# Kernel optimization log

Hardware: AMD Instinct MI355X
Metric: run time of the kernel (lower is better)

## Reference

```python
import jax, jax.numpy as jnp
import numpy as np

N_NODES = 50000
N_EDGES = 800000
C = 128
D_IN = 32
T0, T1 = 25000, 25000
OUT = 16


def setup_inputs() -> dict:
    key = jax.random.key(0)
    ks = jax.random.split(key, 16)
    s_in = 1.0 / np.sqrt(D_IN)
    s_c = 1.0 / np.sqrt(C)
    return {
        "feats0": jax.random.normal(ks[0], (T0, D_IN), jnp.float32),
        "feats1": jax.random.normal(ks[1], (T1, D_IN), jnp.float32),
        "enc_w0": jax.random.normal(ks[2], (D_IN, C), jnp.float32) * s_in,
        "enc_b0": jnp.zeros((C,), jnp.float32),
        "enc_w1": jax.random.normal(ks[3], (D_IN, C), jnp.float32) * s_in,
        "enc_b1": jnp.zeros((C,), jnp.float32),
        "w_self0": jax.random.normal(ks[4], (C, C), jnp.float32) * s_c,
        "w_neigh0": jax.random.normal(ks[5], (C, C), jnp.float32) * s_c,
        "b0": jnp.zeros((C,), jnp.float32),
        "w_self1": jax.random.normal(ks[6], (C, C), jnp.float32) * s_c,
        "w_neigh1": jax.random.normal(ks[7], (C, C), jnp.float32) * s_c,
        "b1": jnp.zeros((C,), jnp.float32),
        "head_w": jax.random.normal(ks[8], (C, OUT), jnp.float32) * s_c,
        "head_b": jnp.zeros((OUT,), jnp.float32),
        "node_row_idx": jax.random.randint(ks[9], (N_NODES,), 0, T0 + T1, jnp.int32),
        "edge_index": jax.random.randint(ks[10], (2, N_EDGES), 0, N_NODES, jnp.int32),
    }


def reference(feats0, feats1, enc_w0, enc_b0, enc_w1, enc_b1,
              w_self0, w_neigh0, b0, w_self1, w_neigh1, b1,
              head_w, head_b, node_row_idx, edge_index):
    # Heterogeneous per-table encoding -> [T0+T1, C]
    x0 = feats0 @ enc_w0 + enc_b0
    x1 = feats1 @ enc_w1 + enc_b1
    x_all = jnp.concatenate([x0, x1], axis=0)
    # Irregular gather: each graph node pulls its table row (vectorized form
    # of the Python loop over index_dict/inverse_index_dict in the original)
    x = x_all[node_row_idx]  # [N, C]

    src, dst = edge_index[0], edge_index[1]
    deg = jnp.maximum(
        jax.ops.segment_sum(jnp.ones((N_EDGES,), x.dtype), dst, num_segments=N_NODES),
        1.0)[:, None]

    # GraphSAGE (mean aggr), 2 layers, ReLU between layers
    for ws, wn, bb, act in ((w_self0, w_neigh0, b0, True),
                            (w_self1, w_neigh1, b1, False)):
        agg = jax.ops.segment_sum(x[src], dst, num_segments=N_NODES) / deg
        x = x @ ws + agg @ wn + bb
        if act:
            x = jax.nn.relu(x)

    return x @ head_w + head_b  # [N, OUT]
```

## Files before the change

kernel.cpp:

```cpp
#include <hip/hip_runtime.h>
#include <hip/hip_bf16.h>

#define N_NODES 50000
#define N_EDGES 800000
#define C 128
#define D_IN 32
#define T0 25000
#define OUT_DIM 16
#define NBUCKETS ((N_NODES + 255) / 256)
#define NB1 512
#define CHUNK1 ((N_EDGES + NB1 - 1) / NB1)
#define ENC_BLOCKS 512
#define HIST_BLOCKS 256
#define PREP_ITEMS (2 * 128 * 256 + 2 * 16 * 128)
#define PREP_BLOCKS ((PREP_ITEMS + 255) / 256)


typedef __attribute__((ext_vector_type(8))) short short8;
typedef __attribute__((ext_vector_type(4))) float f32x4;

__device__ __forceinline__ unsigned short f2bf(float f) {
    union { float f; unsigned int i; } u; u.f = f;
    unsigned int x = u.i;
    unsigned int r = x + 0x7fffu + ((x >> 16) & 1u);
    return (unsigned short)(r >> 16);
}
__device__ __forceinline__ float bf2f(unsigned short h) {
    union { unsigned int i; float f; } u; u.i = ((unsigned int)h) << 16;
    return u.f;
}
__device__ __forceinline__ float lo_f(unsigned int w) {
    union { unsigned int i; float f; } u; u.i = w << 16;
    return u.f;
}
__device__ __forceinline__ float hi_f(unsigned int w) {
    union { unsigned int i; float f; } u; u.i = w & 0xffff0000u;
    return u.f;
}
__device__ __forceinline__ void async16(void* lds, const void* g) {
    __builtin_amdgcn_global_load_lds(
        (const __attribute__((address_space(1))) void*)g,
        (__attribute__((address_space(3))) void*)lds, 16, 0, 0);
}
__device__ __forceinline__ void add8(float* a, uint4 v) {
    a[0] += lo_f(v.x); a[1] += hi_f(v.x);
    a[2] += lo_f(v.y); a[3] += hi_f(v.y);
    a[4] += lo_f(v.z); a[5] += hi_f(v.z);
    a[6] += lo_f(v.w); a[7] += hi_f(v.w);
}

__global__ __launch_bounds__(256) void encode_hist_prep_kernel(
    const float* __restrict__ feats0, const float* __restrict__ feats1,
    const float* __restrict__ w0, const float* __restrict__ b0,
    const float* __restrict__ w1, const float* __restrict__ b1,
    const int* __restrict__ row_idx, unsigned short* __restrict__ xh,
    const int* __restrict__ dst, int* __restrict__ bucket_counts,
    const float* __restrict__ ws0, const float* __restrict__ wn0,
    const float* __restrict__ ws1, const float* __restrict__ wn1,
    const float* __restrict__ hw,
    unsigned short* __restrict__ BT0, unsigned short* __restrict__ BT1,
    unsigned short* __restrict__ hwbh, unsigned short* __restrict__ hwbl)
{
    if (blockIdx.x >= ENC_BLOCKS + HIST_BLOCKS) {
        int idx = (blockIdx.x - ENC_BLOCKS - HIST_BLOCKS) * 256 + threadIdx.x;
        const int per_layer = 128 * 256;
        if (idx < 2 * per_layer) {
            int lyr = idx / per_layer;
            int rem = idx - lyr * per_layer;
            int n = rem >> 8;
            int k = rem & 255;
            int seg = k >> 7;
            int ch = k & 127;
            const float* W = (lyr == 0) ? (seg ? wn0 : ws0)
                                        : (seg ? wn1 : ws1);
            (lyr == 0 ? BT0 : BT1)[(size_t)n * 256 + k] =
                f2bf(W[ch * 128 + n]);
            return;
        }
        int jdx = idx - 2 * per_layer;
        if (jdx >= 2 * 16 * 128) return;
        int plane = jdx >> 11;
        int rem = jdx & 2047;
        int n = rem >> 7;
        int k = rem & 127;
        float v = hw[k * OUT_DIM + n];
        unsigned short hi = f2bf(v);
        (plane ? hwbl : hwbh)[n * 136 + k] = plane ? f2bf(v - bf2f(hi)) : hi;
        return;
    }
    if (blockIdx.x >= ENC_BLOCKS) {
        __shared__ int h[NBUCKETS];
        for (int i = threadIdx.x; i < NBUCKETS; i += 256) h[i] = 0;
        __syncthreads();
        int bid = blockIdx.x - ENC_BLOCKS;
        for (int e = bid * 256 + threadIdx.x; e < N_EDGES;
             e += HIST_BLOCKS * 256)
            atomicAdd(&h[dst[e] >> 8], 1);
        __syncthreads();
        for (int i = threadIdx.x; i < NBUCKETS; i += 256)
            if (h[i]) atomicAdd(&bucket_counts[i], h[i]);
        return;
    }

    __shared__ float sw0[D_IN * C];
    __shared__ float sw1[D_IN * C];
    __shared__ float sb0[C];
    __shared__ float sb1[C];
    for (int i = threadIdx.x; i < D_IN * C; i += blockDim.x) {
        sw0[i] = w0[i];
        sw1[i] = w1[i];
    }
    if (threadIdx.x < C) {
        sb0[threadIdx.x] = b0[threadIdx.x];
        sb1[threadIdx.x] = b1[threadIdx.x];
    }
    __syncthreads();

    const int STEP = ENC_BLOCKS * 16;
    int j = threadIdx.x & 15;
    int ln = threadIdx.x >> 4;
    int n = blockIdx.x * 16 + ln;
    int r = (n < N_NODES) ? row_idx[n] : 0;
    for (; n < N_NODES; n += STEP) {
        int nn = n + STEP;
        int rn = (nn < N_NODES) ? row_idx[nn] : 0;
        const float* f = (r < T0) ? (feats0 + (size_t)r * D_IN)
                                  : (feats1 + (size_t)(r - T0) * D_IN);
        const float* W = (r < T0) ? sw0 : sw1;
        const float* B = (r < T0) ? sb0 : sb1;
        float4 f4[8];
#pragma unroll
        for (int i = 0; i < 8; ++i) f4[i] = ((const float4*)f)[i];
        float acc[8];
#pragma unroll
        for (int cc = 0; cc < 8; ++cc) acc[cc] = B[8 * j + cc];
#pragma unroll
        for (int k = 0; k < D_IN; ++k) {
            float fk = ((const float*)f4)[k];
            float4 wa = *(const float4*)&W[k * C + 8 * j];
            float4 wb = *(const float4*)&W[k * C + 8 * j + 4];
            acc[0] += fk * wa.x; acc[1] += fk * wa.y;
            acc[2] += fk * wa.z; acc[3] += fk * wa.w;
            acc[4] += fk * wb.x; acc[5] += fk * wb.y;
            acc[6] += fk * wb.z; acc[7] += fk * wb.w;
        }
        short8 h8;
#pragma unroll
        for (int cc = 0; cc < 8; ++cc) h8[cc] = (short)f2bf(acc[cc]);
        *(short8*)(xh + (size_t)n * 128 + 8 * j) = h8;
        r = rn;
    }
}

__global__ __launch_bounds__(256) void scanb_kernel(
    const int* __restrict__ bucket_counts, int* __restrict__ bucket_base,
    int* __restrict__ bucket_cursor, int* __restrict__ offsets)
{
    __shared__ int ws[4];
    int t = threadIdx.x;
    int c = (t < NBUCKETS) ? bucket_counts[t] : 0;
    int lane = t & 63, wid = t >> 6;
    int v = c;
#pragma unroll
    for (int off = 1; off < 64; off <<= 1) {
        int s = __shfl_up(v, off, 64);
        if (lane >= off) v += s;
    }
    if (lane == 63) ws[wid] = v;
    __syncthreads();
    if (t == 0) {
        int run = 0;
#pragma unroll
        for (int j = 0; j < 4; ++j) { int s = ws[j]; ws[j] = run; run += s; }
    }
    __syncthreads();
    int excl = ws[wid] + (v - c);
    if (t < NBUCKETS) {
        bucket_base[t] = excl;
        bucket_cursor[t] = excl;
    }
    if (t == 0) {
        bucket_base[NBUCKETS] = N_EDGES;
        offsets[N_NODES] = N_EDGES;
    }
}

__global__ __launch_bounds__(256) void bucket1_kernel(
    const int* __restrict__ src, const int* __restrict__ dst,
    int* __restrict__ bucket_cursor, uint2* __restrict__ pairs)
{
    __shared__ int hist[NBUCKETS];
    __shared__ int base[NBUCKETS];
    __shared__ int cur[NBUCKETS];
    int tid = threadIdx.x;
    for (int i = tid; i < NBUCKETS; i += 256) { hist[i] = 0; cur[i] = 0; }
    __syncthreads();
    int ebeg = blockIdx.x * CHUNK1;
    int eend = ebeg + CHUNK1;
    if (eend > N_EDGES) eend = N_EDGES;
    for (int e = ebeg + tid; e < eend; e += 256)
        atomicAdd(&hist[dst[e] >> 8], 1);
    __syncthreads();
    for (int i = tid; i < NBUCKETS; i += 256)
        if (hist[i] > 0) base[i] = atomicAdd(&bucket_cursor[i], hist[i]);
    __syncthreads();
    for (int e = ebeg + tid; e < eend; e += 256) {
        int d = dst[e];
        int b = d >> 8;
        int pos = base[b] + atomicAdd(&cur[b], 1);
        pairs[pos] = make_uint2((unsigned)src[e], (unsigned)d);
    }
}

__global__ __launch_bounds__(256) void bucket2_kernel(
    const uint2* __restrict__ pairs, const int* __restrict__ bucket_base,
    int* __restrict__ offsets, float* __restrict__ deg,
    int* __restrict__ src_sorted)
{
    __shared__ int cnt[256];
    __shared__ int noff[256];
    __shared__ int cur[256];
    __shared__ int ws[4];
    int b = blockIdx.x;
    int n0 = b << 8;
    int tid = threadIdx.x;
    int bb = bucket_base[b];
    int be = bucket_base[b + 1];
    cnt[tid] = 0;
    cur[tid] = 0;
    __syncthreads();
    for (int e = bb + tid; e < be; e += 256)
        atomicAdd(&cnt[pairs[e].y & 255], 1);
    __syncthreads();
    int c = cnt[tid];
    int lane = tid & 63, wid = tid >> 6;
    int v = c;
#pragma unroll
    for (int off = 1; off < 64; off <<= 1) {
        int s = __shfl_up(v, off, 64);
        if (lane >= off) v += s;
    }
    if (lane == 63) ws[wid] = v;
    __syncthreads();
    if (tid == 0) {
        int run = 0;
#pragma unroll
        for (int j = 0; j < 4; ++j) { int s = ws[j]; ws[j] = run; run += s; }
    }
    __syncthreads();
    int o = bb + ws[wid] + (v - c);
    noff[tid] = o;
    int n = n0 + tid;
    if (n < N_NODES) {
        offsets[n] = o;
        deg[n] = (float)(c > 0 ? c : 1);
    }
    __syncthreads();
    for (int e = bb + tid; e < be; e += 256) {
        uint2 p = pairs[e];
        int local = p.y & 255;
        int pos = noff[local] + atomicAdd(&cur[local], 1);
        src_sorted[pos] = (int)p.x;
    }
}

__global__ __launch_bounds__(256) void aggregate_kernel(
    const unsigned short* __restrict__ xh, const int* __restrict__ offsets,
    const int* __restrict__ src_sorted, const float* __restrict__ deg,
    unsigned short* __restrict__ ah)
{
    int wave = (blockIdx.x * blockDim.x + threadIdx.x) >> 6;
    int lane = threadIdx.x & 63;
    if (wave >= N_NODES) return;
    int h = lane >> 4;
    int u = lane & 15;
    int beg = offsets[wave];
    int end = offsets[wave + 1];
    float acc[8];
#pragma unroll
    for (int j = 0; j < 8; ++j) acc[j] = 0.f;

    for (int e = beg; e < end; e += 32) {
        int idx[8], s[8];
#pragma unroll
        for (int t = 0; t < 8; ++t) {
            idx[t] = e + 4 * t + h;
            int cc = idx[t] < end ? idx[t] : beg;
            s[t] = src_sorted[cc];
        }
        uint4 v[8];
#pragma unroll
        for (int t = 0; t < 8; ++t)
            v[t] = *(const uint4*)(xh + (size_t)s[t] * 128 + u * 8);
#pragma unroll
        for (int t = 0; t < 8; ++t)
            if (idx[t] < end) add8(acc, v[t]);
    }

#pragma unroll
    for (int j = 0; j < 8; ++j) {
        acc[j] += __shfl_xor(acc[j], 16);
        acc[j] += __shfl_xor(acc[j], 32);
    }
    if (lane < 16) {
        float inv = 1.0f / deg[wave];
        short8 hv;
#pragma unroll
        for (int j = 0; j < 8; ++j)
            hv[j] = (short)f2bf(acc[j] * inv);
        *(short8*)(ah + (size_t)wave * 128 + u * 8) = hv;
    }
}

#define BM 128
__global__ __launch_bounds__(512) void gemm_mfma(
    unsigned short* __restrict__ xh, const unsigned short* __restrict__ ah,
    const unsigned short* __restrict__ BT, const float* __restrict__ bias,
    int mode,
    const unsigned short* __restrict__ hwbh,
    const unsigned short* __restrict__ hwbl,
    const float* __restrict__ hb, float* __restrict__ out)
{
    __shared__ uint4 smem4[4096];
    char* As = (char*)smem4;
    char* Bs = (char*)smem4 + 32768;
    __shared__ float bias_s[C];
    __shared__ unsigned short hwh_s[16 * 136];
    __shared__ unsigned short hwl_s[16 * 136];
    __shared__ float hb_s[OUT_DIM];

    int tid = threadIdx.x;
    int w = tid >> 6, l = tid & 63;
    int row0 = blockIdx.x * BM;
    if (tid < C) bias_s[tid] = bias[tid];
    if (mode == 2) {
        for (int i = tid; i < 16 * 136; i += 512) {
            hwh_s[i] = hwbh[i];
            hwl_s[i] = hwbl[i];
        }
        if (tid < OUT_DIM) hb_s[tid] = hb[tid];
    }

    f32x4 acc[2][4];
#pragma unroll
    for (int mt = 0; mt < 2; ++mt)
#pragma unroll
        for (int nt = 0; nt < 4; ++nt)
            acc[mt][nt] = (f32x4)(0.f);

    int wm = w & 3;
    int wn = w >> 2;
    int quad = l >> 4;
    int mrow = l & 15;

    for (int c = 0; c < 2; ++c) {
        const char* abase = (const char*)(c == 0 ? xh : ah);
#pragma unroll
        for (int i = 0; i < 4; ++i) {
            int off = i * 8192 + tid * 16;
            int rl = off >> 8;
            int row = row0 + rl;
            if (row > N_NODES - 1) row = N_NODES - 1;
            int u = ((off >> 4) & 15) ^ (rl & 15);
            async16(As + off, abase + (size_t)row * 256 + u * 16);
        }
#pragma unroll
        for (int i = 0; i < 4; ++i) {
            int off = i * 8192 + tid * 16;
            int n = off >> 8;
            int u = ((off >> 4) & 15) ^ (n & 15);
            async16(Bs + off, (const char*)BT + (size_t)n * 512 + c * 256 + u * 16);
        }
        __syncthreads();
#pragma unroll
        for (int ks = 0; ks < 4; ++ks) {
            int cu = ks * 4 + quad;
            int swz = (cu ^ mrow) * 16;
            short8 a0 = *(const short8*)(As + (wm * 32 + mrow) * 256 + swz);
            short8 a1 = *(const short8*)(As + (wm * 32 + 16 + mrow) * 256 + swz);
            short8 b[4];
#pragma unroll
            for (int nt = 0; nt < 4; ++nt)
                b[nt] = *(const short8*)(Bs + (wn * 64 + nt * 16 + mrow) * 256 + swz);
#pragma unroll
            for (int nt = 0; nt < 4; ++nt) {
                acc[0][nt] = __builtin_amdgcn_mfma_f32_16x16x32_bf16(a0, b[nt], acc[0][nt], 0, 0, 0);
                acc[1][nt] = __builtin_amdgcn_mfma_f32_16x16x32_bf16(a1, b[nt], acc[1][nt], 0, 0, 0);
            }
        }
        __syncthreads();
    }

    char* th = (char*)smem4;
    int relu = (mode == 1);
#pragma unroll
    for (int mt = 0; mt < 2; ++mt)
#pragma unroll
        for (int nt = 0; nt < 4; ++nt) {
            int col = wn * 64 + nt * 16 + mrow;
#pragma unroll
            for (int r = 0; r < 4; ++r) {
                int rl = wm * 32 + mt * 16 + quad * 4 + r;
                float v = acc[mt][nt][r] + bias_s[col];
                if (relu) v = fmaxf(v, 0.f);
                int su = (col >> 3) ^ (rl & 15);
                *(unsigned short*)(th + rl * 256 + su * 16 + (col & 7) * 2) =
                    f2bf(v);
            }
        }
    __syncthreads();

    if (mode == 1) {
#pragma unroll
        for (int i = 0; i < 4; ++i) {
            int off = i * 8192 + tid * 16;
            int rl = off >> 8;
            int su = (((off >> 4) & 15) ^ (rl & 15)) * 16;
            int row = row0 + rl;
            if (row < N_NODES)
                *(uint4*)((char*)xh + (size_t)row * 256 + (off & 255)) =
                    *(const uint4*)(th + rl * 256 + su);
        }
    } else {
        f32x4 hacc = (f32x4)(0.f);
        const unsigned short* Bp[2] = {hwh_s, hwl_s};
#pragma unroll
        for (int ps = 0; ps < 2; ++ps) {
#pragma unroll
            for (int ks = 0; ks < 4; ++ks) {
                int su = ((ks * 4 + quad) ^ mrow) * 16;
                short8 a = *(const short8*)(th + (w * 16 + mrow) * 256 + su);
                short8 b = *(const short8*)((const char*)Bp[ps] +
                                            mrow * 272 + ks * 64 + quad * 16);
                hacc = __builtin_amdgcn_mfma_f32_16x16x32_bf16(a, b, hacc, 0, 0, 0);
            }
        }
        float bb = hb_s[mrow];
#pragma unroll
        for (int r = 0; r < 4; ++r) {
            int grow = row0 + w * 16 + quad * 4 + r;
            if (grow < N_NODES)
                out[(size_t)grow * OUT_DIM + mrow] = hacc[r] + bb;
        }
    }
}

extern "C" void kernel_launch(void* const* d_in, const int* in_sizes, int n_in,
                              void* d_out, int out_size, void* d_ws, size_t ws_size,
                              hipStream_t stream)
{
    const float* feats0 = (const float*)d_in[0];
    const float* feats1 = (const float*)d_in[1];
    const float* enc_w0 = (const float*)d_in[2];
    const float* enc_b0 = (const float*)d_in[3];
    const float* enc_w1 = (const float*)d_in[4];
    const float* enc_b1 = (const float*)d_in[5];
    const float* w_self0 = (const float*)d_in[6];
    const float* w_neigh0 = (const float*)d_in[7];
    const float* b0 = (const float*)d_in[8];
    const float* w_self1 = (const float*)d_in[9];
    const float* w_neigh1 = (const float*)d_in[10];
    const float* b1 = (const float*)d_in[11];
    const float* head_w = (const float*)d_in[12];
    const float* head_b = (const float*)d_in[13];
    const int* node_row_idx = (const int*)d_in[14];
    const int* edge_index = (const int*)d_in[15];
    const int* e_src = edge_index;
    const int* e_dst = edge_index + N_EDGES;

    char* p = (char*)d_ws;
    unsigned short* xh = (unsigned short*)p;  p += (size_t)N_NODES * C * 2;
    unsigned short* ah = (unsigned short*)p;  p += (size_t)N_NODES * C * 2;
    unsigned short* BT0 = (unsigned short*)p; p += (size_t)128 * 256 * 2;
    unsigned short* BT1 = (unsigned short*)p; p += (size_t)128 * 256 * 2;
    unsigned short* hwbh = (unsigned short*)p; p += (size_t)16 * 136 * 2;
    unsigned short* hwbl = (unsigned short*)p; p += (size_t)16 * 136 * 2;
    float* deg = (float*)p;        p += (size_t)N_NODES * 4;
    int* offsets = (int*)p;        p += (size_t)(N_NODES + 8) * 4;
    int* bucket_counts = (int*)p;  p += (size_t)(NBUCKETS + 8) * 4;
    int* bucket_base = (int*)p;    p += (size_t)(NBUCKETS + 8) * 4;
    int* bucket_cursor = (int*)p;  p += (size_t)(NBUCKETS + 8) * 4;
    int* src_sorted = (int*)p;     p += (size_t)N_EDGES * 4;
    uint2* pairs = (uint2*)ah;

    hipMemsetAsync(bucket_counts, 0, (size_t)(NBUCKETS + 8) * 4, stream);

    encode_hist_prep_kernel<<<ENC_BLOCKS + HIST_BLOCKS + PREP_BLOCKS, 256, 0,
                              stream>>>(
        feats0, feats1, enc_w0, enc_b0, enc_w1, enc_b1, node_row_idx, xh,
        e_dst, bucket_counts,
        w_self0, w_neigh0, w_self1, w_neigh1, head_w, BT0, BT1, hwbh, hwbl);

    scanb_kernel<<<1, 256, 0, stream>>>(bucket_counts, bucket_base,
                                        bucket_cursor, offsets);
    bucket1_kernel<<<NB1, 256, 0, stream>>>(e_src, e_dst, bucket_cursor, pairs);
    bucket2_kernel<<<NBUCKETS, 256, 0, stream>>>(pairs, bucket_base, offsets,
                                                 deg, src_sorted);

    aggregate_kernel<<<(N_NODES * 64 + 255) / 256, 256, 0, stream>>>(
        xh, offsets, src_sorted, deg, ah);
    gemm_mfma<<<(N_NODES + BM - 1) / BM, 512, 0, stream>>>(
        xh, ah, BT0, b0, 1, hwbh, hwbl, head_b, (float*)d_out);

    aggregate_kernel<<<(N_NODES * 64 + 255) / 256, 256, 0, stream>>>(
        xh, offsets, src_sorted, deg, ah);
    gemm_mfma<<<(N_NODES + BM - 1) / BM, 512, 0, stream>>>(
        xh, ah, BT1, b1, 2, hwbh, hwbl, head_b, (float*)d_out);
}
```

Measured before the change: 226.0 us.

## Fuse neighbor mean aggregation into the SAGE layer GEMM kernel

The separate aggregate kernel is removed. Each GEMM block now gathers and averages neighbor rows for its 128 nodes directly into shared memory, one wave per 16 nodes, then runs the neighbor-weight MFMA followed by the self-weight MFMA. This drops the write and re-read of the aggregated bf16 buffer and two kernel launches. It also double-buffers x (xh to xnew) so blocks never overwrite rows other blocks are still gathering. The trade-off is a gather phase with only 391 blocks and 16 sequential nodes per wave, which may lower latency hiding compared with the one-wave-per-node kernel, and the pairs buffer now takes extra workspace.

```diff
diff --git a/kernel.cpp b/kernel.cpp
--- a/kernel.cpp
+++ b/kernel.cpp
@@ -264,57 +264,11 @@
     }
 }
 
-__global__ __launch_bounds__(256) void aggregate_kernel(
-    const unsigned short* __restrict__ xh, const int* __restrict__ offsets,
-    const int* __restrict__ src_sorted, const float* __restrict__ deg,
-    unsigned short* __restrict__ ah)
-{
-    int wave = (blockIdx.x * blockDim.x + threadIdx.x) >> 6;
-    int lane = threadIdx.x & 63;
-    if (wave >= N_NODES) return;
-    int h = lane >> 4;
-    int u = lane & 15;
-    int beg = offsets[wave];
-    int end = offsets[wave + 1];
-    float acc[8];
-#pragma unroll
-    for (int j = 0; j < 8; ++j) acc[j] = 0.f;
-
-    for (int e = beg; e < end; e += 32) {
-        int idx[8], s[8];
-#pragma unroll
-        for (int t = 0; t < 8; ++t) {
-            idx[t] = e + 4 * t + h;
-            int cc = idx[t] < end ? idx[t] : beg;
-            s[t] = src_sorted[cc];
-        }
-        uint4 v[8];
-#pragma unroll
-        for (int t = 0; t < 8; ++t)
-            v[t] = *(const uint4*)(xh + (size_t)s[t] * 128 + u * 8);
-#pragma unroll
-        for (int t = 0; t < 8; ++t)
-            if (idx[t] < end) add8(acc, v[t]);
-    }
-
-#pragma unroll
-    for (int j = 0; j < 8; ++j) {
-        acc[j] += __shfl_xor(acc[j], 16);
-        acc[j] += __shfl_xor(acc[j], 32);
-    }
-    if (lane < 16) {
-        float inv = 1.0f / deg[wave];
-        short8 hv;
-#pragma unroll
-        for (int j = 0; j < 8; ++j)
-            hv[j] = (short)f2bf(acc[j] * inv);
-        *(short8*)(ah + (size_t)wave * 128 + u * 8) = hv;
-    }
-}
-
 #define BM 128
-__global__ __launch_bounds__(512) void gemm_mfma(
-    unsigned short* __restrict__ xh, const unsigned short* __restrict__ ah,
+__global__ __launch_bounds__(512, 4) void gemm_fused(
+    const unsigned short* __restrict__ xin, unsigned short* __restrict__ xout,
+    const int* __restrict__ offsets, const int* __restrict__ src_sorted,
+    const float* __restrict__ deg,
     const unsigned short* __restrict__ BT, const float* __restrict__ bias,
     int mode,
     const unsigned short* __restrict__ hwbh,
@@ -341,55 +295,122 @@
         if (tid < OUT_DIM) hb_s[tid] = hb[tid];
     }
 
-    f32x4 acc[2][4];
-#pragma unroll
-    for (int mt = 0; mt < 2; ++mt)
-#pragma unroll
-        for (int nt = 0; nt < 4; ++nt)
-            acc[mt][nt] = (f32x4)(0.f);
-
     int wm = w & 3;
     int wn = w >> 2;
     int quad = l >> 4;
     int mrow = l & 15;
-
-    for (int c = 0; c < 2; ++c) {
-        const char* abase = (const char*)(c == 0 ? xh : ah);
-#pragma unroll
-        for (int i = 0; i < 4; ++i) {
-            int off = i * 8192 + tid * 16;
-            int rl = off >> 8;
-            int row = row0 + rl;
-            if (row > N_NODES - 1) row = N_NODES - 1;
-            int u = ((off >> 4) & 15) ^ (rl & 15);
-            async16(As + off, abase + (size_t)row * 256 + u * 16);
-        }
-#pragma unroll
-        for (int i = 0; i < 4; ++i) {
-            int off = i * 8192 + tid * 16;
-            int n = off >> 8;
-            int u = ((off >> 4) & 15) ^ (n & 15);
-            async16(Bs + off, (const char*)BT + (size_t)n * 512 + c * 256 + u * 16);
-        }
-        __syncthreads();
-#pragma unroll
-        for (int ks = 0; ks < 4; ++ks) {
-            int cu = ks * 4 + quad;
-            int swz = (cu ^ mrow) * 16;
-            short8 a0 = *(const short8*)(As + (wm * 32 + mrow) * 256 + swz);
-            short8 a1 = *(const short8*)(As + (wm * 32 + 16 + mrow) * 256 + swz);
-            short8 b[4];
-#pragma unroll
-            for (int nt = 0; nt < 4; ++nt)
-                b[nt] = *(const short8*)(Bs + (wn * 64 + nt * 16 + mrow) * 256 + swz);
-#pragma unroll
-            for (int nt = 0; nt < 4; ++nt) {
-                acc[0][nt] = __builtin_amdgcn_mfma_f32_16x16x32_bf16(a0, b[nt], acc[0][nt], 0, 0, 0);
-                acc[1][nt] = __builtin_amdgcn_mfma_f32_16x16x32_bf16(a1, b[nt], acc[1][nt], 0, 0, 0);
+    int h = l >> 4;
+    int u = l & 15;
+
+#pragma unroll
+    for (int i = 0; i < 4; ++i) {
+        int off = i * 8192 + tid * 16;
+        int n = off >> 8;
+        int uu = ((off >> 4) & 15) ^ (n & 15);
+        async16(Bs + off, (const char*)BT + (size_t)n * 512 + 256 + uu * 16);
+    }
+
+    for (int i = 0; i < 16; ++i) {
+        int rl = w * 16 + i;
+        int node = row0 + rl;
+        if (node > N_NODES - 1) node = N_NODES - 1;
+        int beg = offsets[node];
+        int end = offsets[node + 1];
+        float acc[8];
+#pragma unroll
+        for (int j = 0; j < 8; ++j) acc[j] = 0.f;
+        for (int e = beg; e < end; e += 32) {
+            int idx[8], s[8];
+#pragma unroll
+            for (int t = 0; t < 8; ++t) {
+                idx[t] = e + 4 * t + h;
+                int cc = idx[t] < end ? idx[t] : beg;
+                s[t] = src_sorted[cc];
             }
-        }
-        __syncthreads();
-    }
+            uint4 v[8];
+#pragma unroll
+            for (int t = 0; t < 8; ++t)
+                v[t] = *(const uint4*)(xin + (size_t)s[t] * 128 + u * 8);
+#pragma unroll
+            for (int t = 0; t < 8; ++t)
+                if (idx[t] < end) add8(acc, v[t]);
+        }
+#pragma unroll
+        for (int j = 0; j < 8; ++j) {
+            acc[j] += __shfl_xor(acc[j], 16);
+            acc[j] += __shfl_xor(acc[j], 32);
+        }
+        if (l < 16) {
+            float inv = 1.0f / deg[node];
+            short8 hv;
+#pragma unroll
+            for (int j = 0; j < 8; ++j)
+                hv[j] = (short)f2bf(acc[j] * inv);
+            int su = u ^ (rl & 15);
+            *(short8*)(As + rl * 256 + su * 16) = hv;
+        }
+    }
+    __syncthreads();
+
+    f32x4 acc[2][4];
+#pragma unroll
+    for (int mt = 0; mt < 2; ++mt)
+#pragma unroll
+        for (int nt = 0; nt < 4; ++nt)
+            acc[mt][nt] = (f32x4)(0.f);
+
+#pragma unroll
+    for (int ks = 0; ks < 4; ++ks) {
+        int cu = ks * 4 + quad;
+        int swz = (cu ^ mrow) * 16;
+        short8 a0 = *(const short8*)(As + (wm * 32 + mrow) * 256 + swz);
+        short8 a1 = *(const short8*)(As + (wm * 32 + 16 + mrow) * 256 + swz);
+        short8 b[4];
+#pragma unroll
+        for (int nt = 0; nt < 4; ++nt)
+            b[nt] = *(const short8*)(Bs + (wn * 64 + nt * 16 + mrow) * 256 + swz);
+#pragma unroll
+        for (int nt = 0; nt < 4; ++nt) {
+            acc[0][nt] = __builtin_amdgcn_mfma_f32_16x16x32_bf16(a0, b[nt], acc[0][nt], 0, 0, 0);
+            acc[1][nt] = __builtin_amdgcn_mfma_f32_16x16x32_bf16(a1, b[nt], acc[1][nt], 0, 0, 0);
+        }
+    }
+    __syncthreads();
+
+#pragma unroll
+    for (int i = 0; i < 4; ++i) {
+        int off = i * 8192 + tid * 16;
+        int rl = off >> 8;
+        int row = row0 + rl;
+        if (row > N_NODES - 1) row = N_NODES - 1;
+        int uu = ((off >> 4) & 15) ^ (rl & 15);
+        async16(As + off, (const char*)xin + (size_t)row * 256 + uu * 16);
+    }
+#pragma unroll
+    for (int i = 0; i < 4; ++i) {
+        int off = i * 8192 + tid * 16;
+        int n = off >> 8;
+        int uu = ((off >> 4) & 15) ^ (n & 15);
+        async16(Bs + off, (const char*)BT + (size_t)n * 512 + uu * 16);
+    }
+    __syncthreads();
+#pragma unroll
+    for (int ks = 0; ks < 4; ++ks) {
+        int cu = ks * 4 + quad;
+        int swz = (cu ^ mrow) * 16;
+        short8 a0 = *(const short8*)(As + (wm * 32 + mrow) * 256 + swz);
+        short8 a1 = *(const short8*)(As + (wm * 32 + 16 + mrow) * 256 + swz);
+        short8 b[4];
+#pragma unroll
+        for (int nt = 0; nt < 4; ++nt)
+            b[nt] = *(const short8*)(Bs + (wn * 64 + nt * 16 + mrow) * 256 + swz);
+#pragma unroll
+        for (int nt = 0; nt < 4; ++nt) {
+            acc[0][nt] = __builtin_amdgcn_mfma_f32_16x16x32_bf16(a0, b[nt], acc[0][nt], 0, 0, 0);
+            acc[1][nt] = __builtin_amdgcn_mfma_f32_16x16x32_bf16(a1, b[nt], acc[1][nt], 0, 0, 0);
+        }
+    }
+    __syncthreads();
 
     char* th = (char*)smem4;
     int relu = (mode == 1);
@@ -418,7 +439,7 @@
             int su = (((off >> 4) & 15) ^ (rl & 15)) * 16;
             int row = row0 + rl;
             if (row < N_NODES)
-                *(uint4*)((char*)xh + (size_t)row * 256 + (off & 255)) =
+                *(uint4*)((char*)xout + (size_t)row * 256 + (off & 255)) =
                     *(const uint4*)(th + rl * 256 + su);
         }
     } else {
@@ -469,10 +490,10 @@
     const int* e_dst = edge_index + N_EDGES;
 
     char* p = (char*)d_ws;
-    unsigned short* xh = (unsigned short*)p;  p += (size_t)N_NODES * C * 2;
-    unsigned short* ah = (unsigned short*)p;  p += (size_t)N_NODES * C * 2;
-    unsigned short* BT0 = (unsigned short*)p; p += (size_t)128 * 256 * 2;
-    unsigned short* BT1 = (unsigned short*)p; p += (size_t)128 * 256 * 2;
+    unsigned short* xh = (unsigned short*)p;   p += (size_t)N_NODES * C * 2;
+    unsigned short* xnew = (unsigned short*)p; p += (size_t)N_NODES * C * 2;
+    unsigned short* BT0 = (unsigned short*)p;  p += (size_t)128 * 256 * 2;
+    unsigned short* BT1 = (unsigned short*)p;  p += (size_t)128 * 256 * 2;
     unsigned short* hwbh = (unsigned short*)p; p += (size_t)16 * 136 * 2;
     unsigned short* hwbl = (unsigned short*)p; p += (size_t)16 * 136 * 2;
     float* deg = (float*)p;        p += (size_t)N_NODES * 4;
@@ -481,7 +502,7 @@
     int* bucket_base = (int*)p;    p += (size_t)(NBUCKETS + 8) * 4;
     int* bucket_cursor = (int*)p;  p += (size_t)(NBUCKETS + 8) * 4;
     int* src_sorted = (int*)p;     p += (size_t)N_EDGES * 4;
-    uint2* pairs = (uint2*)ah;
+    uint2* pairs = (uint2*)p;      p += (size_t)N_EDGES * 8;
 
     hipMemsetAsync(bucket_counts, 0, (size_t)(NBUCKETS + 8) * 4, stream);
 
@@ -497,13 +518,11 @@
     bucket2_kernel<<<NBUCKETS, 256, 0, stream>>>(pairs, bucket_base, offsets,
                                                  deg, src_sorted);
 
-    aggregate_kernel<<<(N_NODES * 64 + 255) / 256, 256, 0, stream>>>(
-        xh, offsets, src_sorted, deg, ah);
-    gemm_mfma<<<(N_NODES + BM - 1) / BM, 512, 0, stream>>>(
-        xh, ah, BT0, b0, 1, hwbh, hwbl, head_b, (float*)d_out);
-
-    aggregate_kernel<<<(N_NODES * 64 + 255) / 256, 256, 0, stream>>>(
-        xh, offsets, src_sorted, deg, ah);
-    gemm_mfma<<<(N_NODES + BM - 1) / BM, 512, 0, stream>>>(
-        xh, ah, BT1, b1, 2, hwbh, hwbl, head_b, (float*)d_out);
-}
+    gemm_fused<<<(N_NODES + BM - 1) / BM, 512, 0, stream>>>(
+        xh, xnew, offsets, src_sorted, deg, BT0, b0, 1,
+        hwbh, hwbl, head_b, (float*)d_out);
+
+    gemm_fused<<<(N_NODES + BM - 1) / BM, 512, 0, stream>>>(
+        xnew, nullptr, offsets, src_sorted, deg, BT1, b1, 2,
+        hwbh, hwbl, head_b, (float*)d_out);
+}
```

After: 247.9 us. 1.1x slower.
